# Optimization experiments

Measured on AMD Instinct MI355X. Metric: run time of the kernel, lower is better.

The kernel has to match this reference:

```python
import jax, jax.numpy as jnp
import numpy as np
from jax import lax

# Mamba2 block (training path: mamba_split_conv1d_scan_combined equivalent)
B = 2; L = 2048; D_MODEL = 2048
INTER = 4096          # ssm_intermediate_size
NH = 64; HD = INTER // NH   # num_heads, head_dim
N = 128               # ssm_state_size
G = 1                 # n_groups
K = 4                 # conv kernel
CS = 256              # chunk size
EPS = 1e-5
CONV_DIM = INTER + 2 * G * N          # 4352
PROJ_DIM = INTER + CONV_DIM + NH      # 8512


def setup_inputs() -> dict:
    key = jax.random.key(0)
    ks = jax.random.split(key, 4)
    std = 0.02
    return {
        "hidden_states": jax.random.normal(ks[0], (B, L, D_MODEL), jnp.float32),
        "W_in": jax.random.normal(ks[1], (PROJ_DIM, D_MODEL), jnp.float32) * std,
        "conv_w": jax.random.normal(ks[2], (CONV_DIM, K), jnp.float32) * std,
        "conv_b": jnp.zeros((CONV_DIM,), jnp.float32),
        "dt_bias": jnp.ones((NH,), jnp.float32),
        "A_log": jnp.log(jnp.arange(1, NH + 1, dtype=jnp.float32)),
        "D": jnp.ones((NH,), jnp.float32),
        "norm_w": jnp.ones((INTER,), jnp.float32),
        "W_out": jax.random.normal(ks[3], (D_MODEL, INTER), jnp.float32) * std,
    }


def _segsum(x):
    # x: [..., s] -> [..., s, s] lower-triangular cumulative sums (masked with -inf)
    s = x.shape[-1]
    xc = jnp.cumsum(x, axis=-1)
    d = xc[..., :, None] - xc[..., None, :]
    return jnp.where(jnp.tril(jnp.ones((s, s), dtype=bool)), d, -jnp.inf)


def _forward(hidden_states, W_in, conv_w, conv_b, dt_bias, A_log, D, norm_w, W_out):
    proj = hidden_states @ W_in.T                              # [B,L,PROJ_DIM]
    gate = proj[..., :INTER]
    hBC = proj[..., INTER:INTER + CONV_DIM]
    dt = proj[..., INTER + CONV_DIM:]                          # [B,L,NH]

    # causal depthwise conv1d + silu
    xc = hBC.transpose(0, 2, 1)                                # [B,CONV_DIM,L]
    y = lax.conv_general_dilated(
        xc, conv_w[:, None, :], (1,), [(K - 1, 0)],
        dimension_numbers=("NCH", "OIH", "NCH"), feature_group_count=CONV_DIM)
    hBC = jax.nn.silu(y + conv_b[None, :, None]).transpose(0, 2, 1)

    x = hBC[..., :INTER].reshape(B, L, NH, HD)
    Bm = hBC[..., INTER:INTER + G * N].reshape(B, L, G, N)
    Cm = hBC[..., INTER + G * N:].reshape(B, L, G, N)

    dtv = jax.nn.softplus(dt + dt_bias)                        # [B,L,NH], dt_softplus=True
    A = -jnp.exp(A_log)                                        # [NH]

    # ---- chunked selective scan (SSD) ----
    c = L // CS
    xch = x.reshape(B, c, CS, NH, HD)
    dtch = dtv.reshape(B, c, CS, NH)
    Bh = jnp.repeat(Bm.reshape(B, c, CS, G, N), NH // G, axis=3)   # [B,c,s,NH,N]
    Ch = jnp.repeat(Cm.reshape(B, c, CS, G, N), NH // G, axis=3)

    dA = (dtch * A).transpose(0, 3, 1, 2)                      # [B,NH,c,s]
    Acum = jnp.cumsum(dA, axis=-1)                             # [B,NH,c,s]
    Lmat = jnp.exp(_segsum(dA))                                # [B,NH,c,s,s]

    # within-chunk (diagonal block) output
    Ydiag = jnp.einsum("bcihn,bcjhn,bhcij,bcjh,bcjhp->bcihp",
                       Ch, Bh, Lmat, dtch, xch)

    # per-chunk states
    decay_states = jnp.exp(Acum[..., -1:] - Acum)              # [B,NH,c,s]
    states = jnp.einsum("bcjhn,bhcj,bcjh,bcjhp->bchpn",
                        Bh, decay_states, dtch, xch)           # [B,c,NH,HD,N]

    # inter-chunk recurrence (scan over chunks)
    chunk_decay = jnp.exp(Acum[..., -1])                       # [B,NH,c]

    def step(carry, inp):
        st, dec = inp
        new = dec[:, :, None, None] * carry + st
        return new, carry                                      # emit state at chunk start

    init = jnp.zeros((B, NH, HD, N), dtype=x.dtype)
    _, prev = lax.scan(step, init,
                       (states.transpose(1, 0, 2, 3, 4), chunk_decay.transpose(2, 0, 1)))
    prev = prev.transpose(1, 0, 2, 3, 4)                       # [B,c,NH,HD,N]

    Yoff = jnp.einsum("bcihn,bchpn,bhci->bcihp", Ch, prev, jnp.exp(Acum))

    Y = (Ydiag + Yoff).reshape(B, L, NH, HD) + x * D[None, None, :, None]
    yout = Y.reshape(B, L, INTER)

    # gated RMSNorm (norm_before_gate=False): gate first, then normalize
    yout = yout * jax.nn.silu(gate)
    yout = yout * lax.rsqrt(jnp.mean(yout * yout, axis=-1, keepdims=True) + EPS) * norm_w
    return yout @ W_out.T                                      # [B,L,D_MODEL]


def reference(hidden_states, W_in, conv_w, conv_b, dt_bias, A_log, D, norm_w, W_out):
    return _forward(hidden_states, W_in, conv_w, conv_b, dt_bias, A_log, D, norm_w, W_out)
```

## Files before the change

kernel.cpp:

```cpp
#include <hip/hip_runtime.h>
#include <cstdint>

typedef __bf16 bf16;
typedef __bf16 bf16x8 __attribute__((ext_vector_type(8)));
typedef __bf16 bf16x4 __attribute__((ext_vector_type(4)));
typedef float  f32x4  __attribute__((ext_vector_type(4)));

#define BQ     2
#define LQ     2048
#define DMODEL 2048
#define INTER  4096
#define NH     64
#define HD     64
#define NS     128
#define CS     256
#define NC     8
#define CONVD  4352
#define PROJD  8512
#define PROJP  8576
#define PROJW  8704
#define MTOT   4096
#define EPSF   1e-5f
#define LOG2E  1.44269504088896f

__device__ __forceinline__ void async_ld16(const bf16* g, bf16* l) {
  __builtin_amdgcn_global_load_lds(
      (__attribute__((address_space(1))) void*)(uintptr_t)g,
      (__attribute__((address_space(3))) void*)l, 16, 0, 0);
}

__device__ __forceinline__ float siluf(float x) { return x / (1.f + expf(-x)); }

#define SB()    __builtin_amdgcn_sched_barrier(0)
#define HWBAR() __builtin_amdgcn_s_barrier()
#define LGKM0() asm volatile("s_waitcnt lgkmcnt(0)" ::: "memory")

__global__ void cast4_k(const float* __restrict__ in, bf16* __restrict__ out, long n4) {
  long i = (long)blockIdx.x * 256 + threadIdx.x;
  if (i >= n4) return;
  float4 v = ((const float4*)in)[i];
  bf16x4 o; o[0] = (bf16)v.x; o[1] = (bf16)v.y; o[2] = (bf16)v.z; o[3] = (bf16)v.w;
  ((bf16x4*)out)[i] = o;
}

__global__ void cast_pad_win_k(const float* __restrict__ W, bf16* __restrict__ out) {
  long i = (long)blockIdx.x * 256 + threadIdx.x;
  long tot = (long)PROJW * (DMODEL / 4);
  if (i >= tot) return;
  long row = i / (DMODEL / 4);
  long k4  = i % (DMODEL / 4);
  bf16x4 o;
  if (row < PROJD) {
    float4 v = ((const float4*)W)[row * (DMODEL / 4) + k4];
    o[0] = (bf16)v.x; o[1] = (bf16)v.y; o[2] = (bf16)v.z; o[3] = (bf16)v.w;
  } else {
    o[0] = o[1] = o[2] = o[3] = (bf16)0.f;
  }
  ((bf16x4*)out)[i] = o;
}


template<int R0>
__device__ __forceinline__ void ldfrag(bf16x8 (&dst)[4][2], const char* base,
                                       int r16, int quad, int xr) {
  #pragma unroll
  for (int f = 0; f < 4; ++f)
    #pragma unroll
    for (int kk = 0; kk < 2; ++kk)
      dst[f][kk] = *(const bf16x8*)(base + (((R0 + f) * 16 + r16) << 7)
                                         + ((((kk << 2) + quad) ^ xr) << 4));
}

template<int M0, int I0>
__device__ __forceinline__ void qmfma(f32x4 (&acc)[8][4], const bf16x8 (&ar)[4][2],
                                      const bf16x8 (&b)[4][2]) {
  #pragma unroll
  for (int mm = 0; mm < 2; ++mm)
    #pragma unroll
    for (int nf = 0; nf < 4; ++nf)
      #pragma unroll
      for (int kk = 0; kk < 2; ++kk)
        acc[M0 + mm][nf] = __builtin_amdgcn_mfma_f32_16x16x32_bf16(
            ar[I0 + mm][kk], b[nf][kk], acc[M0 + mm][nf], 0, 0, 0);
}

__global__ __launch_bounds__(512, 2) void gemm8(
    const bf16* __restrict__ A, const bf16* __restrict__ W,
    bf16* __restrict__ Cb, float* __restrict__ Cf,
    int M, int Nn, int Ntiles, int K, int KS, int outf32)
{
  __shared__ int4 lds4[8192];
  char* lds = (char*)lds4;
  const int tid  = threadIdx.x;
  const int w    = tid >> 6;
  const int l    = tid & 63;
  const int wm   = w >> 2;
  const int wn   = w & 3;
  const int quad = l >> 4;
  const int r16  = l & 15;
  const int xr   = r16 & 7;

  const int Mtiles  = M >> 8;
  const int tilesMN = Mtiles * Ntiles;
  const int nwg = tilesMN * KS;
  int bid = blockIdx.x;
  int sid = ((nwg & 7) == 0) ? ((bid & 7) * (nwg >> 3) + (bid >> 3)) : bid;
  const int ks  = sid / tilesMN;
  const int rem = sid - ks * tilesMN;
  const int by = rem % Mtiles;
  const int bx = rem / Mtiles;
  const long tm = (long)by << 8;
  const long tn = (long)bx << 8;
  const int  NT = K / (64 * KS);
  const long kbase = (long)ks * (K / KS);

  const int srow = w * 8 + (l >> 3);
  const int scg  = (l & 7) ^ ((l >> 3) & 7);
  const bf16* Ab = A + (tm + srow) * K + kbase + scg * 8;
  const bf16* Wb = W + (tn + srow) * K + kbase + scg * 8;

  auto stage = [&](int tile, int part) {
    if (tile < NT) {
      const bf16* s = (part < 2 ? Ab : Wb) + (long)((part & 1) * 128) * K + (long)tile * 64;
      char* d = lds + ((tile & 1) << 16) + (part << 14) + (w << 10);
      async_ld16(s, (bf16*)d);
      async_ld16(s + (long)K * 64, (bf16*)(d + 8192));
    }
  };

  stage(0, 0); stage(0, 1); stage(0, 2); stage(0, 3);
  stage(1, 2); stage(1, 0); stage(1, 1);
  SB();
  asm volatile("s_waitcnt vmcnt(6)" ::: "memory");
  SB();
  HWBAR();
  SB();

  f32x4 acc[8][4] = {};

  for (int T = 0; T < NT; ++T) {
    const int bsel = (T & 1) << 16;
    const char* as = lds + bsel + (wm << 14);
    const char* bs = lds + bsel + 32768 + ((wn >> 1) << 14) + ((wn & 1) << 13);
    bf16x8 a0[4][2], a1[4][2], b[4][2];

    ldfrag<0>(b,  bs, r16, quad, xr);
    ldfrag<0>(a0, as, r16, quad, xr);
    stage(T + 1, 3);
    SB(); HWBAR(); LGKM0(); SB();
    __builtin_amdgcn_s_setprio(1);
    qmfma<0, 0>(acc, a0, b);
    __builtin_amdgcn_s_setprio(0);
    SB(); HWBAR(); SB();

    ldfrag<4>(a1, as, r16, quad, xr);
    stage(T + 2, 2);
    SB(); HWBAR(); LGKM0(); SB();
    __builtin_amdgcn_s_setprio(1);
    qmfma<2, 2>(acc, a0, b);
    __builtin_amdgcn_s_setprio(0);
    SB(); HWBAR(); SB();

    stage(T + 2, 0);
    SB(); HWBAR(); LGKM0(); SB();
    __builtin_amdgcn_s_setprio(1);
    qmfma<4, 0>(acc, a1, b);
    __builtin_amdgcn_s_setprio(0);
    SB(); HWBAR(); SB();

    stage(T + 2, 1);
    SB(); HWBAR(); LGKM0(); SB();
    __builtin_amdgcn_s_setprio(1);
    qmfma<6, 2>(acc, a1, b);
    __builtin_amdgcn_s_setprio(0);
    SB();
    if (T + 2 < NT) { asm volatile("s_waitcnt vmcnt(6)" ::: "memory"); }
    else            { asm volatile("s_waitcnt vmcnt(0)" ::: "memory"); }
    SB(); HWBAR(); SB();
  }

  const long cbase = (long)ks * M * Nn;
  #pragma unroll
  for (int mf = 0; mf < 8; ++mf)
    #pragma unroll
    for (int nf = 0; nf < 4; ++nf) {
      long r0 = tm + wm * 128 + mf * 16 + quad * 4;
      long cc = tn + wn * 64 + nf * 16 + r16;
      if (cc < Nn) {
        #pragma unroll
        for (int reg = 0; reg < 4; ++reg) {
          long idx = (r0 + reg) * (long)Nn + cc;
          if (outf32) Cf[cbase + idx] = acc[mf][nf][reg];
          else        Cb[idx] = (bf16)acc[mf][nf][reg];
        }
      }
    }
}

__global__ void addred_k(const float* __restrict__ P, float* __restrict__ out, long n4) {
  long i = (long)blockIdx.x * 256 + threadIdx.x;
  if (i >= n4) return;
  float4 a = ((const float4*)P)[i];
  float4 b = ((const float4*)P)[i + n4];
  float4 r; r.x = a.x + b.x; r.y = a.y + b.y; r.z = a.z + b.z; r.w = a.w + b.w;
  ((float4*)out)[i] = r;
}

__global__ void conv_silu_k(const bf16* __restrict__ proj,
                            const float* __restrict__ conv_w,
                            const float* __restrict__ conv_b,
                            bf16* __restrict__ xconv,
                            bf16* __restrict__ Bmb, bf16* __restrict__ Cmb,
                            bf16* __restrict__ Bt)
{
  int ch = blockIdx.x * 256 + threadIdx.x;
  if (ch >= CONVD) return;
  long bl = blockIdx.y;
  int l = (int)(bl & (LQ - 1));
  float acc = conv_b[ch];
  #pragma unroll
  for (int t = 0; t < 4; ++t) {
    int ls = l - 3 + t;
    if (ls >= 0)
      acc += (float)proj[(bl - 3 + t) * PROJP + INTER + ch] * conv_w[ch * 4 + t];
  }
  float y = siluf(acc);
  if (ch < INTER) {
    xconv[bl * INTER + ch] = (bf16)y;
  } else if (ch < INTER + NS) {
    int n = ch - INTER;
    Bmb[bl * NS + n] = (bf16)y;
    int b = (int)(bl >> 11), ci = l >> 8, j = l & 255;
    Bt[(((long)(b * NC + ci) * NS) + n) * CS + j] = (bf16)y;
  } else {
    Cmb[bl * NS + (ch - INTER - NS)] = (bf16)y;
  }
}

__global__ __launch_bounds__(CS) void dt_prep_k(
    const bf16* __restrict__ proj, const float* __restrict__ dt_bias,
    const float* __restrict__ A_log,
    float* __restrict__ dtv, float* __restrict__ acum, float* __restrict__ cdec)
{
  int bx = blockIdx.x;
  int ci = bx & 7;
  int bh = bx >> 3;
  int h  = bh & 63;
  int b  = bh >> 6;
  int i  = threadIdx.x;
  long pos = (long)b * LQ + ci * CS + i;
  float draw = (float)proj[pos * PROJP + INTER + CONVD + h] + dt_bias[h];
  float dv = draw > 20.f ? draw : log1pf(expf(draw));
  float Ah = -expf(A_log[h]);
  __shared__ float s[CS];
  s[i] = dv * Ah;
  __syncthreads();
  for (int off = 1; off < CS; off <<= 1) {
    float t = (i >= off) ? s[i - off] : 0.f;
    __syncthreads();
    s[i] += t;
    __syncthreads();
  }
  long base = (long)bx * CS;
  dtv[base + i]  = dv;
  acum[base + i] = s[i];
  if (i == 0) cdec[bx] = expf(s[CS - 1]);
}

__global__ __launch_bounds__(256) void gmat_k(
    const bf16* __restrict__ Cmb, const bf16* __restrict__ Bmb, float* __restrict__ Gnt)
{
  int q  = blockIdx.x;
  int bc = blockIdx.y;
  long bl0 = (long)(bc >> 3) * LQ + (bc & 7) * CS;
  int wave = threadIdx.x >> 6, lane = threadIdx.x & 63;
  int quad = lane >> 4, r16 = lane & 15;
  int i0 = (q >> 1) * 128 + (wave >> 1) * 64;
  int j0 = (q & 1)  * 128 + (wave & 1)  * 64;

  f32x4 acc[4][4] = {};
  #pragma unroll
  for (int kt = 0; kt < 4; ++kt) {
    int k0 = kt * 32 + quad * 8;
    bf16x8 af[4], bfv[4];
    #pragma unroll
    for (int it = 0; it < 4; ++it)
      af[it] = *(const bf16x8*)&Cmb[(bl0 + i0 + it * 16 + r16) * NS + k0];
    #pragma unroll
    for (int nt = 0; nt < 4; ++nt)
      bfv[nt] = *(const bf16x8*)&Bmb[(bl0 + j0 + nt * 16 + r16) * NS + k0];
    #pragma unroll
    for (int it = 0; it < 4; ++it)
      #pragma unroll
      for (int nt = 0; nt < 4; ++nt)
        acc[it][nt] = __builtin_amdgcn_mfma_f32_16x16x32_bf16(af[it], bfv[nt], acc[it][nt], 0, 0, 0);
  }
  #pragma unroll
  for (int it = 0; it < 4; ++it)
    #pragma unroll
    for (int nt = 0; nt < 4; ++nt)
      #pragma unroll
      for (int reg = 0; reg < 4; ++reg) {
        int i = i0 + it * 16 + quad * 4 + reg;
        int j = j0 + nt * 16 + r16;
        Gnt[((long)bc * CS + i) * CS + j] = acc[it][nt][reg];
      }
}

__global__ __launch_bounds__(256) void states_k(
    const bf16* __restrict__ xconv, const bf16* __restrict__ Bt,
    const float* __restrict__ dtv, const float* __restrict__ acum,
    bf16* __restrict__ st)
{
  int bx = blockIdx.x;
  int h = bx & 63, bc = bx >> 6;
  int b = bc >> 3, ci = bc & 7;
  long bl0 = (long)b * LQ + ci * CS;
  long abase = ((long)(b * NH + h) * NC + ci) * CS;
  int t = threadIdx.x;
  int wave = t >> 6, lane = t & 63, quad = lane >> 4, r16 = lane & 15;

  __shared__ bf16 Xt[64][264];
  __shared__ float ws[CS];
  __shared__ float ac_s[CS];
  ac_s[t] = acum[abase + t];
  __syncthreads();
  float alast = ac_s[CS - 1];
  ws[t] = expf(alast - ac_s[t]) * dtv[abase + t];
  {
    int col = t & 63, grp = t >> 6;
    for (int r = 0; r < 64; ++r) {
      int j = grp * 64 + r;
      Xt[col][j] = xconv[(bl0 + j) * INTER + h * HD + col];
    }
  }
  __syncthreads();

  const bf16* btb = &Bt[(long)bc * NS * CS];
  f32x4 acc[8] = {};
  int p = wave * 16 + r16;
  #pragma unroll
  for (int kt = 0; kt < 8; ++kt) {
    int k0 = kt * 32 + quad * 8;
    bf16x8 xv = *(const bf16x8*)&Xt[p][k0];
    float w8[8];
    *(float4*)&w8[0] = *(const float4*)&ws[k0];
    *(float4*)&w8[4] = *(const float4*)&ws[k0 + 4];
    bf16x8 af;
    #pragma unroll
    for (int jj = 0; jj < 8; ++jj) af[jj] = (bf16)((float)xv[jj] * w8[jj]);
    #pragma unroll
    for (int nt = 0; nt < 8; ++nt) {
      bf16x8 bfv = *(const bf16x8*)&btb[(nt * 16 + r16) * CS + k0];
      acc[nt] = __builtin_amdgcn_mfma_f32_16x16x32_bf16(af, bfv, acc[nt], 0, 0, 0);
    }
  }
  #pragma unroll
  for (int nt = 0; nt < 8; ++nt)
    #pragma unroll
    for (int reg = 0; reg < 4; ++reg) {
      int prow = wave * 16 + quad * 4 + reg;
      int n = nt * 16 + r16;
      st[((long)bx * HD + prow) * NS + n] = (bf16)acc[nt][reg];
    }
}

__global__ void scan_k(bf16* __restrict__ st, const float* __restrict__ cdec)
{
  long t = (long)blockIdx.x * 256 + threadIdx.x;
  int n = (int)(t & 127);
  int p = (int)((t >> 7) & 63);
  int h = (int)((t >> 13) & 63);
  int b = (int)(t >> 19);
  float carry = 0.f;
  for (int ci = 0; ci < NC; ++ci) {
    long idx = (((long)(b * NC + ci) * NH + h) * HD + p) * NS + n;
    float v = (float)st[idx];
    st[idx] = (bf16)carry;
    carry = cdec[(b * NH + h) * NC + ci] * carry + v;
  }
}

#define XTP 392
__global__ __launch_bounds__(256) void ymix_k(
    const bf16* __restrict__ xconv, const float* __restrict__ Gnt,
    const bf16* __restrict__ prev, const bf16* __restrict__ Cmb,
    const float* __restrict__ dtv, const float* __restrict__ acum,
    const float* __restrict__ Dp, bf16* __restrict__ Y)
{
  int bx = blockIdx.x;
  int h = bx & 63, bc = bx >> 6;
  int b = bc >> 3, ci = bc & 7;
  long bl0 = (long)b * LQ + ci * CS;
  long abase = ((long)(b * NH + h) * NC + ci) * CS;
  int t = threadIdx.x;
  int wave = t >> 6, lane = t & 63;
  int quad = lane >> 4, r16 = lane & 15;
  int iw = wave * 64;

  __shared__ bf16 Xt[64][XTP];
  __shared__ float a2s[CS], dts[CS], eas[CS];

  {
    float ac = acum[abase + t];
    a2s[t] = ac * LOG2E;
    dts[t] = dtv[abase + t];
    eas[t] = expf(ac);
  }
  {
    int col = t & 63, grp = t >> 6;
    for (int r = 0; r < 64; ++r) {
      int j = grp * 64 + r;
      Xt[col][j] = xconv[(bl0 + j) * INTER + h * HD + col];
    }
  }
  for (int r = 0; r < 32; ++r) {
    int idx = t + r * 256;
    int n = idx & 127, p = idx >> 7;
    Xt[p][256 + n] = prev[((long)bx * HD + p) * NS + n];
  }
  __syncthreads();

  f32x4 acc[4][4] = {};

  for (int kt = 0; kt < 12; ++kt) {
    int k0 = kt * 32;
    bool cpart = (k0 >= 256);
    if (!cpart && k0 > iw + 63) continue;

    bf16x8 bfrag[4];
    #pragma unroll
    for (int nt = 0; nt < 4; ++nt)
      bfrag[nt] = *(const bf16x8*)&Xt[nt * 16 + r16][k0 + quad * 8];

    if (!cpart) {
      int j0 = k0 + quad * 8;
      float dt8[8], a28[8];
      *(float4*)&dt8[0] = *(const float4*)&dts[j0];
      *(float4*)&dt8[4] = *(const float4*)&dts[j0 + 4];
      *(float4*)&a28[0] = *(const float4*)&a2s[j0];
      *(float4*)&a28[4] = *(const float4*)&a2s[j0 + 4];
      #pragma unroll
      for (int it = 0; it < 4; ++it) {
        if (k0 > iw + it * 16 + 15) continue;
        int i = iw + it * 16 + r16;
        float a2i = a2s[i];
        const float* gp = &Gnt[((long)bc * CS + i) * CS + j0];
        float g[8];
        *(float4*)&g[0] = *(const float4*)gp;
        *(float4*)&g[4] = *(const float4*)(gp + 4);
        bf16x8 af;
        #pragma unroll
        for (int jj = 0; jj < 8; ++jj) {
          float v = g[jj] * dt8[jj] * exp2f(a2i - a28[jj]);
          v = (j0 + jj <= i) ? v : 0.f;
          af[jj] = (bf16)v;
        }
        #pragma unroll
        for (int nt = 0; nt < 4; ++nt)
          acc[it][nt] = __builtin_amdgcn_mfma_f32_16x16x32_bf16(af, bfrag[nt], acc[it][nt], 0, 0, 0);
      }
    } else {
      int n0 = k0 - 256 + quad * 8;
      #pragma unroll
      for (int it = 0; it < 4; ++it) {
        int i = iw + it * 16 + r16;
        float e = eas[i];
        bf16x8 cv = *(const bf16x8*)&Cmb[(bl0 + i) * NS + n0];
        bf16x8 af;
        #pragma unroll
        for (int jj = 0; jj < 8; ++jj)
          af[jj] = (bf16)(e * (float)cv[jj]);
        #pragma unroll
        for (int nt = 0; nt < 4; ++nt)
          acc[it][nt] = __builtin_amdgcn_mfma_f32_16x16x32_bf16(af, bfrag[nt], acc[it][nt], 0, 0, 0);
      }
    }
  }

  float Dh = Dp[h];
  #pragma unroll
  for (int it = 0; it < 4; ++it)
    #pragma unroll
    for (int nt = 0; nt < 4; ++nt) {
      int i0 = iw + it * 16 + quad * 4;
      int p  = nt * 16 + r16;
      bf16x4 xv = *(const bf16x4*)&Xt[p][i0];
      #pragma unroll
      for (int reg = 0; reg < 4; ++reg) {
        float v = acc[it][nt][reg] + Dh * (float)xv[reg];
        Y[(bl0 + i0 + reg) * INTER + h * HD + p] = (bf16)v;
      }
    }
}

__global__ __launch_bounds__(256) void norm_k(
    bf16* __restrict__ Y, const bf16* __restrict__ proj,
    const float* __restrict__ norm_w)
{
  long bl = blockIdx.x;
  int t = threadIdx.x;
  __shared__ float yb[INTER];
  __shared__ float red[256];
  float ss = 0.f;
  for (int r = 0; r < 16; ++r) {
    int ch = t + r * 256;
    float g = (float)proj[bl * PROJP + ch];
    float yv = (float)Y[bl * INTER + ch] * siluf(g);
    yb[ch] = yv;
    ss += yv * yv;
  }
  red[t] = ss;
  __syncthreads();
  for (int s = 128; s > 0; s >>= 1) {
    if (t < s) red[t] += red[t + s];
    __syncthreads();
  }
  float scale = rsqrtf(red[0] / (float)INTER + EPSF);
  for (int r = 0; r < 16; ++r) {
    int ch = t + r * 256;
    Y[bl * INTER + ch] = (bf16)(yb[ch] * scale * norm_w[ch]);
  }
}

extern "C" void kernel_launch(void* const* d_in, const int* in_sizes, int n_in,
                              void* d_out, int out_size, void* d_ws, size_t ws_size,
                              hipStream_t stream)
{
  (void)in_sizes; (void)n_in; (void)out_size; (void)ws_size;
  const float* hidden  = (const float*)d_in[0];
  const float* W_in    = (const float*)d_in[1];
  const float* conv_w  = (const float*)d_in[2];
  const float* conv_b  = (const float*)d_in[3];
  const float* dt_bias = (const float*)d_in[4];
  const float* A_log   = (const float*)d_in[5];
  const float* Dp      = (const float*)d_in[6];
  const float* norm_w  = (const float*)d_in[7];
  const float* W_out   = (const float*)d_in[8];
  float* out = (float*)d_out;

  char* ws    = (char*)d_ws;
  bf16* projb = (bf16*)(ws);
  char* base2 = ws + 70254592;
  bf16*  hb    = (bf16*)(base2);
  bf16*  winb  = (bf16*)(base2 + 16777216);
  bf16*  xconv = (bf16*)(base2);
  bf16*  st    = (bf16*)(base2 + 33554432);
  float* Gnt   = (float*)(base2 + 50331648);
  bf16*  Bmb   = (bf16*)(base2 + 54525952);
  bf16*  Cmb   = (bf16*)(base2 + 55574528);
  float* dtv   = (float*)(base2 + 56623104);
  float* acum  = (float*)(base2 + 57671680);
  float* cdec  = (float*)(base2 + 58720256);
  bf16*  Bt    = (bf16*)(base2 + 58724352);
  bf16*  Yb    = xconv;
  bf16*  woutb = st;

  cast4_k<<<dim3((unsigned)((MTOT * (long)DMODEL / 4 + 255) / 256)), 256, 0, stream>>>(
      hidden, hb, (long)MTOT * DMODEL / 4);
  cast_pad_win_k<<<dim3((unsigned)(((long)PROJW * (DMODEL / 4) + 255) / 256)), 256, 0, stream>>>(
      W_in, winb);
  gemm8<<<dim3((PROJW / 256) * (MTOT / 256)), 512, 0, stream>>>(
      hb, winb, projb, nullptr, MTOT, PROJP, PROJW / 256, DMODEL, 1, 0);

  conv_silu_k<<<dim3(CONVD / 256, MTOT), 256, 0, stream>>>(
      projb, conv_w, conv_b, xconv, Bmb, Cmb, Bt);
  dt_prep_k<<<dim3(BQ * NH * NC), CS, 0, stream>>>(
      projb, dt_bias, A_log, dtv, acum, cdec);
  gmat_k<<<dim3(4, BQ * NC), 256, 0, stream>>>(Cmb, Bmb, Gnt);
  states_k<<<dim3(BQ * NC * NH), 256, 0, stream>>>(xconv, Bt, dtv, acum, st);
  scan_k<<<dim3(BQ * NH * HD * NS / 256), 256, 0, stream>>>(st, cdec);
  ymix_k<<<dim3(BQ * NC * NH), 256, 0, stream>>>(
      xconv, Gnt, st, Cmb, dtv, acum, Dp, Yb);

  cast4_k<<<dim3((unsigned)((DMODEL * (long)INTER / 4 + 255) / 256)), 256, 0, stream>>>(
      W_out, woutb, (long)DMODEL * INTER / 4);
  norm_k<<<dim3(MTOT), 256, 0, stream>>>(Yb, projb, norm_w);
  gemm8<<<dim3((DMODEL / 256) * (MTOT / 256) * 2), 512, 0, stream>>>(
      Yb, woutb, nullptr, (float*)projb, MTOT, DMODEL, DMODEL / 256, INTER, 2, 1);
  addred_k<<<dim3((unsigned)((MTOT * (long)DMODEL / 4 + 255) / 256)), 256, 0, stream>>>(
      (const float*)projb, out, (long)MTOT * DMODEL / 4);
}
```

Measured before the change: 663.7 us.

## Rebalance GEMM K-loop into four A-slice phases with reordered async staging

```diff
diff --git a/kernel.cpp b/kernel.cpp
--- a/kernel.cpp
+++ b/kernel.cpp
@@ -61,8 +61,8 @@
 
 
 template<int R0>
-__device__ __forceinline__ void ldfrag(bf16x8 (&dst)[4][2], const char* base,
-                                       int r16, int quad, int xr) {
+__device__ __forceinline__ void ldB4(bf16x8 (&dst)[4][2], const char* base,
+                                     int r16, int quad, int xr) {
   #pragma unroll
   for (int f = 0; f < 4; ++f)
     #pragma unroll
@@ -71,17 +71,28 @@
                                          + ((((kk << 2) + quad) ^ xr) << 4));
 }
 
-template<int M0, int I0>
-__device__ __forceinline__ void qmfma(f32x4 (&acc)[8][4], const bf16x8 (&ar)[4][2],
+template<int R0>
+__device__ __forceinline__ void ldA2(bf16x8 (&dst)[8][2], const char* base,
+                                     int r16, int quad, int xr) {
+  #pragma unroll
+  for (int f = 0; f < 2; ++f)
+    #pragma unroll
+    for (int kk = 0; kk < 2; ++kk)
+      dst[R0 + f][kk] = *(const bf16x8*)(base + (((R0 + f) * 16 + r16) << 7)
+                                              + ((((kk << 2) + quad) ^ xr) << 4));
+}
+
+template<int M0>
+__device__ __forceinline__ void qmfma(f32x4 (&acc)[8][4], const bf16x8 (&a)[8][2],
                                       const bf16x8 (&b)[4][2]) {
   #pragma unroll
-  for (int mm = 0; mm < 2; ++mm)
+  for (int kk = 0; kk < 2; ++kk)
     #pragma unroll
     for (int nf = 0; nf < 4; ++nf)
       #pragma unroll
-      for (int kk = 0; kk < 2; ++kk)
+      for (int mm = 0; mm < 2; ++mm)
         acc[M0 + mm][nf] = __builtin_amdgcn_mfma_f32_16x16x32_bf16(
-            ar[I0 + mm][kk], b[nf][kk], acc[M0 + mm][nf], 0, 0, 0);
+            a[M0 + mm][kk], b[nf][kk], acc[M0 + mm][nf], 0, 0, 0);
 }
 
 __global__ __launch_bounds__(512, 2) void gemm8(
@@ -129,12 +140,10 @@
   };
 
   stage(0, 0); stage(0, 1); stage(0, 2); stage(0, 3);
-  stage(1, 2); stage(1, 0); stage(1, 1);
-  SB();
-  asm volatile("s_waitcnt vmcnt(6)" ::: "memory");
+  stage(1, 2); stage(1, 3);
+  asm volatile("s_waitcnt vmcnt(4)" ::: "memory");
   SB();
   HWBAR();
-  SB();
 
   f32x4 acc[8][4] = {};
 
@@ -142,41 +151,43 @@
     const int bsel = (T & 1) << 16;
     const char* as = lds + bsel + (wm << 14);
     const char* bs = lds + bsel + 32768 + ((wn >> 1) << 14) + ((wn & 1) << 13);
-    bf16x8 a0[4][2], a1[4][2], b[4][2];
-
-    ldfrag<0>(b,  bs, r16, quad, xr);
-    ldfrag<0>(a0, as, r16, quad, xr);
-    stage(T + 1, 3);
-    SB(); HWBAR(); LGKM0(); SB();
+    bf16x8 a[8][2], b[4][2];
+
+    ldB4<0>(b, bs, r16, quad, xr);
+    ldA2<0>(a, as, r16, quad, xr);
+    stage(T + 1, 0);
+    HWBAR(); LGKM0(); SB();
     __builtin_amdgcn_s_setprio(1);
-    qmfma<0, 0>(acc, a0, b);
+    qmfma<0>(acc, a, b);
     __builtin_amdgcn_s_setprio(0);
-    SB(); HWBAR(); SB();
-
-    ldfrag<4>(a1, as, r16, quad, xr);
+    HWBAR();
+
+    ldA2<2>(a, as, r16, quad, xr);
+    stage(T + 1, 1);
+    HWBAR(); LGKM0(); SB();
+    __builtin_amdgcn_s_setprio(1);
+    qmfma<2>(acc, a, b);
+    __builtin_amdgcn_s_setprio(0);
+    HWBAR();
+
+    ldA2<4>(a, as, r16, quad, xr);
     stage(T + 2, 2);
-    SB(); HWBAR(); LGKM0(); SB();
+    HWBAR(); LGKM0(); SB();
     __builtin_amdgcn_s_setprio(1);
-    qmfma<2, 2>(acc, a0, b);
+    qmfma<4>(acc, a, b);
     __builtin_amdgcn_s_setprio(0);
-    SB(); HWBAR(); SB();
-
-    stage(T + 2, 0);
-    SB(); HWBAR(); LGKM0(); SB();
+    HWBAR();
+
+    ldA2<6>(a, as, r16, quad, xr);
+    stage(T + 2, 3);
+    HWBAR(); LGKM0(); SB();
     __builtin_amdgcn_s_setprio(1);
-    qmfma<4, 0>(acc, a1, b);
+    qmfma<6>(acc, a, b);
     __builtin_amdgcn_s_setprio(0);
-    SB(); HWBAR(); SB();
-
-    stage(T + 2, 1);
-    SB(); HWBAR(); LGKM0(); SB();
-    __builtin_amdgcn_s_setprio(1);
-    qmfma<6, 2>(acc, a1, b);
-    __builtin_amdgcn_s_setprio(0);
+    if (T + 2 < NT) { asm volatile("s_waitcnt vmcnt(4)" ::: "memory"); }
+    else            { asm volatile("s_waitcnt vmcnt(0)" ::: "memory"); }
     SB();
-    if (T + 2 < NT) { asm volatile("s_waitcnt vmcnt(6)" ::: "memory"); }
-    else            { asm volatile("s_waitcnt vmcnt(0)" ::: "memory"); }
-    SB(); HWBAR(); SB();
+    HWBAR();
   }
 
   const long cbase = (long)ks * M * Nn;
```

After: 657.9 us. Within noise of the previous version (-0.9%).
